# Optimization experiments

Measured on AMD Instinct MI355X. Metric: run time of the kernel, lower is better.

The kernel has to match this reference:

```python
import jax, jax.numpy as jnp
import numpy as np

B, S, D, H = 2, 2048, 1024, 16
DH = D // H  # head_dim = 64


def setup_inputs() -> dict:
    key = jax.random.key(0)
    ks = jax.random.split(key, 12)
    sd = 0.02
    return {
        "query": jax.random.normal(ks[0], (B, S, D), jnp.float32),
        "value": jax.random.normal(ks[1], (B, S, D), jnp.float32),
        "Wq": jax.random.normal(ks[2], (D, D), jnp.float32) * sd,
        "bq": jnp.zeros((D,), jnp.float32),
        "Wk": jax.random.normal(ks[3], (D, DH), jnp.float32) * sd,
        "bk": jnp.zeros((DH,), jnp.float32),
        "Wv": jax.random.normal(ks[4], (D, DH), jnp.float32) * sd,
        "bv": jnp.zeros((DH,), jnp.float32),
        "Wo": jax.random.normal(ks[5], (D, D), jnp.float32) * sd,
        "bo": jnp.zeros((D,), jnp.float32),
    }


def reference(query, value, Wq, bq, Wk, bk, Wv, bv, Wo, bo):
    b, s, d = query.shape
    # per-head queries: (B, H, S, DH)
    Q = (query @ Wq + bq).reshape(b, s, H, DH).transpose(0, 2, 1, 3)
    # single shared K/V head: (B, S, DH)
    K = value @ Wk + bk
    V = value @ Wv + bv
    scale = 1.0 / jnp.sqrt(jnp.asarray(DH, Q.dtype))
    # broadcast shared K over all query heads: (B, H, S, S)
    scores = jnp.einsum("bhsd,btd->bhst", Q, K) * scale
    weights = jax.nn.softmax(scores, axis=-1)
    # (B, H, S, DH)
    attn = jnp.einsum("bhst,btd->bhsd", weights, V)
    concat = attn.transpose(0, 2, 1, 3).reshape(b, s, d)
    return concat @ Wo + bo
```

## Files before the change

### kernel.cpp

```cpp
#include <hip/hip_runtime.h>
#include <hip/hip_bf16.h>
#include <cstdint>

#define S_LEN 2048
#define D_MODEL 1024
#define NHEAD 16
#define DHEAD 64
#define BATCH 2

typedef __attribute__((ext_vector_type(4))) __bf16 bf16x4v;
typedef __attribute__((ext_vector_type(8))) __bf16 bf16x8v;
typedef __attribute__((ext_vector_type(16))) float f32x16;
typedef const __attribute__((address_space(1))) uint32_t gu32;
typedef __attribute__((address_space(3))) uint32_t lu32;

#define QSCALE 0.18033688011112042f

__device__ __forceinline__ int perm4(int gidx) {
    return (gidx & ~3) | ((gidx & 1) << 1) | ((gidx >> 1) & 1);
}
__device__ __forceinline__ int permk(int k) {
    return (k & ~12) | ((k & 4) << 1) | ((k & 8) >> 1);
}

__global__ __launch_bounds__(256) void cvt_f32_bf16(
    const float* __restrict__ in, __hip_bfloat16* __restrict__ out, int n4)
{
    const int i = blockIdx.x * 256 + threadIdx.x;
    if (i < n4) {
        const float4 v = reinterpret_cast<const float4*>(in)[i];
        bf16x4v o = { (__bf16)v.x, (__bf16)v.y, (__bf16)v.z, (__bf16)v.w };
        *reinterpret_cast<bf16x4v*>(out + (size_t)perm4(i) * 4) = o;
    }
}

__global__ __launch_bounds__(256) void wtrans(
    const float* __restrict__ W, __hip_bfloat16* __restrict__ T, int wcols, int trowoff)
{
    __shared__ float ld[32][33];
    const int tid = threadIdx.x;
    const int bx = blockIdx.x, by = blockIdx.y;
    const int jj = tid & 31;
#pragma unroll
    for (int ii = 0; ii < 4; ++ii) {
        const int rr = (tid >> 5) * 4 + ii;
        ld[rr][jj] = W[(size_t)(by * 32 + rr) * wcols + bx * 32 + jj];
    }
    __syncthreads();
#pragma unroll
    for (int ii = 0; ii < 4; ++ii) {
        const int rr = (tid >> 5) * 4 + ii;
        T[(size_t)(trowoff + bx * 32 + rr) * 1024 + by * 32 + permk(jj)] =
            __float2bfloat16(ld[jj][rr]);
    }
}

template<bool FUSED, bool PERMC, typename OutT>
__global__ __launch_bounds__(512, 1) void gemm_mfma(
    const __hip_bfloat16* __restrict__ Ahi, const __hip_bfloat16* __restrict__ Alo,
    const __hip_bfloat16* __restrict__ Bhi,
    const float* __restrict__ bias, OutT* __restrict__ C, float oscale)
{
    constexpr int NT = 16;
    constexpr int LDSZ = FUSED ? 98304 : 65536;
    constexpr int BUFSZ = FUSED ? 49152 : 32768;
    __shared__ __align__(16) char lds[LDSZ];

    const int tid = threadIdx.x;
    const int w = tid >> 6, lane = tid & 63;
    const int g = lane >> 5, r = lane & 31;
    const int wr = w >> 2, wc = w & 3;
    const int lin = blockIdx.y * 8 + blockIdx.x;
    const int swz = (lin & 7) * 32 + (lin >> 3);
    const int rowBase = (swz >> 3) * 128;
    const int colBase = (swz & 7) * 128;

    auto stage = [&](int buf, int t) {
        const int kk = t * 64;
        char* dst = lds + buf * BUFSZ;
#pragma unroll
        for (int j = 0; j < 2; ++j) {
            const int oo  = j * 8192 + tid * 16;
            const int row = oo >> 7;
            const int cb  = (oo & 127) ^ ((row & 7) << 4);
            __builtin_amdgcn_global_load_lds(
                (gu32*)((const char*)Ahi + (size_t)(rowBase + row) * 2048 + kk * 2 + cb),
                (lu32*)(dst + oo), 16, 0, 0);
            if (FUSED)
                __builtin_amdgcn_global_load_lds(
                    (gu32*)((const char*)Alo + (size_t)(rowBase + row) * 2048 + kk * 2 + cb),
                    (lu32*)(dst + 16384 + oo), 16, 0, 0);
            __builtin_amdgcn_global_load_lds(
                (gu32*)((const char*)Bhi + (size_t)(colBase + row) * 2048 + kk * 2 + cb),
                (lu32*)(dst + (FUSED ? 32768 : 16384) + oo), 16, 0, 0);
        }
    };

    f32x16 acc[2];
#pragma unroll
    for (int i = 0; i < 16; ++i) { acc[0][i] = 0.f; acc[1][i] = 0.f; }

    stage(0, 0);

    for (int t = 0; t < NT; ++t) {
        const int cur = t & 1;
        if (t < NT - 1) {
            stage(cur ^ 1, t + 1);
            if (FUSED) { asm volatile("s_waitcnt vmcnt(6)" ::: "memory"); }
            else       { asm volatile("s_waitcnt vmcnt(4)" ::: "memory"); }
        } else {
            asm volatile("s_waitcnt vmcnt(0)" ::: "memory");
        }
        asm volatile("s_barrier" ::: "memory");

        const char* ahb = lds + cur * BUFSZ;
        const char* alb = ahb + 16384;
        const char* bb  = ahb + (FUSED ? 32768 : 16384);

        __builtin_amdgcn_s_setprio(1);
#pragma unroll
        for (int ks = 0; ks < 4; ++ks) {
            bf16x8v a[2], bfr;
#pragma unroll
            for (int mt = 0; mt < 2; ++mt) {
                const int rowl = wr * 64 + mt * 32 + r;
                const int sz = (rowl & 7) << 4;
                a[mt] = *reinterpret_cast<const bf16x8v*>(
                    ahb + rowl * 128 + ((ks * 32 + g * 16) ^ sz));
            }
            {
                const int rowl = wc * 32 + r;
                const int sz = (rowl & 7) << 4;
                bfr = *reinterpret_cast<const bf16x8v*>(
                    bb + rowl * 128 + ((ks * 32 + g * 16) ^ sz));
            }
#pragma unroll
            for (int mt = 0; mt < 2; ++mt)
                acc[mt] = __builtin_amdgcn_mfma_f32_32x32x16_bf16(a[mt], bfr, acc[mt], 0, 0, 0);
            if (FUSED) {
                bf16x8v a2[2];
#pragma unroll
                for (int mt = 0; mt < 2; ++mt) {
                    const int rowl = wr * 64 + mt * 32 + r;
                    const int sz = (rowl & 7) << 4;
                    a2[mt] = *reinterpret_cast<const bf16x8v*>(
                        alb + rowl * 128 + ((ks * 32 + g * 16) ^ sz));
                }
#pragma unroll
                for (int mt = 0; mt < 2; ++mt)
                    acc[mt] = __builtin_amdgcn_mfma_f32_32x32x16_bf16(a2[mt], bfr, acc[mt], 0, 0, 0);
            }
        }
        __builtin_amdgcn_s_setprio(0);
        asm volatile("s_barrier" ::: "memory");
    }

    const int col = colBase + wc * 32 + r;
    const int colp = PERMC ? permk(col) : col;
    const float bv = bias[col];
#pragma unroll
    for (int mt = 0; mt < 2; ++mt)
#pragma unroll
        for (int reg = 0; reg < 16; ++reg) {
            const int row = rowBase + wr * 64 + mt * 32 + (reg & 3) + 8 * (reg >> 2) + 4 * g;
            C[(size_t)row * 1024 + colp] = static_cast<OutT>((acc[mt][reg] + bv) * oscale);
        }
}

__global__ __launch_bounds__(256) void proj_kv_mfma(
    const __hip_bfloat16* __restrict__ Vbf,
    const __hip_bfloat16* __restrict__ Wkvt,
    const float* __restrict__ bk, const float* __restrict__ bv,
    __hip_bfloat16* __restrict__ Kb,
    __hip_bfloat16* __restrict__ Vt)
{
    __shared__ __align__(16) char lds[40960];
    const int tid = threadIdx.x;
    const int w = tid >> 6, lane = tid & 63;
    const int g = lane >> 5, r = lane & 31;
    const int rowBase = blockIdx.x * 32;

    auto stage = [&](int buf, int t) {
        const int kk = t * 64;
        char* dst = lds + buf * 20480;
        {
            const int oo  = tid * 16;
            const int row = oo >> 7;
            const int cb  = (oo & 127) ^ ((row & 7) << 4);
            __builtin_amdgcn_global_load_lds(
                (gu32*)((const char*)Vbf + (size_t)(rowBase + row) * 2048 + kk * 2 + cb),
                (lu32*)(dst + oo), 16, 0, 0);
        }
#pragma unroll
        for (int j = 0; j < 4; ++j) {
            const int oo  = j * 4096 + tid * 16;
            const int row = oo >> 7;
            const int cb  = (oo & 127) ^ ((row & 7) << 4);
            __builtin_amdgcn_global_load_lds(
                (gu32*)((const char*)Wkvt + (size_t)row * 2048 + kk * 2 + cb),
                (lu32*)(dst + 4096 + oo), 16, 0, 0);
        }
    };

    f32x16 acc;
#pragma unroll
    for (int i = 0; i < 16; ++i) acc[i] = 0.f;

    stage(0, 0);

    for (int t = 0; t < 16; ++t) {
        const int cur = t & 1;
        if (t < 15) {
            stage(cur ^ 1, t + 1);
            asm volatile("s_waitcnt vmcnt(5)" ::: "memory");
        } else {
            asm volatile("s_waitcnt vmcnt(0)" ::: "memory");
        }
        asm volatile("s_barrier" ::: "memory");

        const char* ab = lds + cur * 20480;
        const char* bb = ab + 4096;

#pragma unroll
        for (int ks = 0; ks < 4; ++ks) {
            const int sza = (r & 7) << 4;
            bf16x8v af = *reinterpret_cast<const bf16x8v*>(
                ab + r * 128 + ((ks * 32 + g * 16) ^ sza));
            bf16x8v bf = *reinterpret_cast<const bf16x8v*>(
                bb + (w * 32 + r) * 128 + ((ks * 32 + g * 16) ^ sza));
            acc = __builtin_amdgcn_mfma_f32_32x32x16_bf16(af, bf, acc, 0, 0, 0);
        }
        asm volatile("s_barrier" ::: "memory");
    }

    __syncthreads();
    float* ep = reinterpret_cast<float*>(lds);
#pragma unroll
    for (int reg = 0; reg < 16; ++reg) {
        const int m = (reg & 3) + 8 * (reg >> 2) + 4 * g;
        ep[m * 132 + w * 32 + r] = acc[reg];
    }
    __syncthreads();

    {
        const int m  = tid >> 3;
        const int g0 = (tid & 7) * 2;
#pragma unroll
        for (int j = 0; j < 2; ++j) {
            const int gsrc = g0 + j;
            bf16x4v o4;
#pragma unroll
            for (int i2 = 0; i2 < 4; ++i2)
                o4[i2] = (__bf16)(ep[m * 132 + gsrc * 4 + i2] + bk[gsrc * 4 + i2]);
            *reinterpret_cast<bf16x4v*>(
                Kb + (size_t)(rowBase + m) * 64 + perm4(gsrc) * 4) = o4;
        }
    }
    {
        const int vc = tid >> 2;
        const int g0 = (tid & 3) * 2;
        const int batch = rowBase >> 11;
        const float bvv = bv[vc];
#pragma unroll
        for (int j = 0; j < 2; ++j) {
            const int gsrc = g0 + j;
            bf16x4v o4;
#pragma unroll
            for (int i2 = 0; i2 < 4; ++i2)
                o4[i2] = (__bf16)(ep[(gsrc * 4 + i2) * 132 + 64 + vc] + bvv);
            *reinterpret_cast<bf16x4v*>(
                Vt + ((size_t)(batch * 64 + vc)) * 2048 + (rowBase & 2047) + perm4(gsrc) * 4) = o4;
        }
    }
}

__global__ __launch_bounds__(256, 2) void mqa_attn_mfma(
    const __hip_bfloat16* __restrict__ Qbf,
    const __hip_bfloat16* __restrict__ Kbf,
    const __hip_bfloat16* __restrict__ Vt,
    __hip_bfloat16* __restrict__ Ahi,
    __hip_bfloat16* __restrict__ Alo)
{
    __shared__ __align__(16) char lds[65536];

    const int bh = blockIdx.y, b = bh >> 4, h = bh & 15;
    const int qt = blockIdx.x;
    const int tid = threadIdx.x;
    const int w = tid >> 6, lane = tid & 63;
    const int g = lane >> 5, q = lane & 31;

    bf16x8v qf[4];
    {
        const __hip_bfloat16* qp =
            Qbf + ((size_t)(b * S_LEN + qt * 128 + w * 32 + q)) * D_MODEL + h * DHEAD;
#pragma unroll
        for (int ks = 0; ks < 4; ++ks)
            qf[ks] = *reinterpret_cast<const bf16x8v*>(qp + ks * 16 + g * 8);
    }

    const bf16x8v onesf = {(__bf16)1.f, (__bf16)1.f, (__bf16)1.f, (__bf16)1.f,
                           (__bf16)1.f, (__bf16)1.f, (__bf16)1.f, (__bf16)1.f};

    const char* kbase = (const char*)Kbf + (size_t)b * S_LEN * DHEAD * 2;
    const char* vbase = (const char*)Vt + (size_t)b * DHEAD * S_LEN * 2;

    auto stage = [&](int buf, int t0) {
        char* dst = lds + buf * 16384;
#pragma unroll
        for (int j = 0; j < 2; ++j) {
            const int oo = j * 4096 + tid * 16;
            const int rr = oo >> 7;
            const int cc = (oo & 127) ^ ((rr & 7) << 4);
            __builtin_amdgcn_global_load_lds(
                (gu32*)(kbase + (size_t)(t0 + rr) * 128 + cc),
                (lu32*)(dst + oo), 16, 0, 0);
            __builtin_amdgcn_global_load_lds(
                (gu32*)(vbase + (size_t)rr * (S_LEN * 2) + t0 * 2 + cc),
                (lu32*)(dst + 8192 + oo), 16, 0, 0);
        }
    };

    f32x16 oacc[2], oacc_l;
#pragma unroll
    for (int i = 0; i < 16; ++i) { oacc[0][i] = 0.f; oacc[1][i] = 0.f; oacc_l[i] = 0.f; }

    auto qkt = [&](f32x16 (&SD)[2], int buf) {
#pragma unroll
        for (int i = 0; i < 16; ++i) { SD[0][i] = 0.f; SD[1][i] = 0.f; }
        const char* kb_ = lds + buf * 16384;
        __builtin_amdgcn_s_setprio(1);
#pragma unroll
        for (int mt = 0; mt < 2; ++mt) {
            const int key = mt * 32 + q;
            const char* krow = kb_ + key * 128;
            const int swz = (key & 7) << 4;
#pragma unroll
            for (int ks = 0; ks < 4; ++ks) {
                bf16x8v af = *reinterpret_cast<const bf16x8v*>(
                    krow + ((ks * 32 + g * 16) ^ swz));
                SD[mt] = __builtin_amdgcn_mfma_f32_32x32x16_bf16(af, qf[ks], SD[mt], 0, 0, 0);
            }
        }
        __builtin_amdgcn_s_setprio(0);
    };

    auto smpv = [&](f32x16 (&SD)[2], int buf) {
#pragma unroll
        for (int mt = 0; mt < 2; ++mt)
#pragma unroll
            for (int r2 = 0; r2 < 16; ++r2)
                SD[mt][r2] = exp2f(SD[mt][r2]);

        bf16x8v pf[4];
#pragma unroll
        for (int ks = 0; ks < 4; ++ks)
#pragma unroll
            for (int e2 = 0; e2 < 8; ++e2)
                pf[ks][e2] = (__bf16)SD[ks >> 1][(ks & 1) * 8 + e2];

        const char* vb_ = lds + buf * 16384 + 8192;
        __builtin_amdgcn_s_setprio(1);
#pragma unroll
        for (int mt = 0; mt < 2; ++mt) {
            const int drow = mt * 32 + q;
            const char* vrow = vb_ + drow * 128;
            const int swz = (drow & 7) << 4;
#pragma unroll
            for (int ks = 0; ks < 4; ++ks) {
                bf16x8v af = *reinterpret_cast<const bf16x8v*>(
                    vrow + ((ks * 32 + g * 16) ^ swz));
                oacc[mt] = __builtin_amdgcn_mfma_f32_32x32x16_bf16(af, pf[ks], oacc[mt], 0, 0, 0);
            }
        }
#pragma unroll
        for (int ks = 0; ks < 4; ++ks)
            oacc_l = __builtin_amdgcn_mfma_f32_32x32x16_bf16(onesf, pf[ks], oacc_l, 0, 0, 0);
        __builtin_amdgcn_s_setprio(0);
    };

    f32x16 sA[2], sB[2];

    stage(0, 0); stage(1, 64); stage(2, 128);
    asm volatile("s_waitcnt vmcnt(8)" ::: "memory");
    asm volatile("s_barrier" ::: "memory");
    qkt(sA, 0);

#define BODY(SB_, TILE_, BQ_, BP_, CUR, NXT, VMCSTR, DOSTAGE)               \
    {                                                                        \
        asm volatile("s_waitcnt vmcnt(" VMCSTR ")" ::: "memory");            \
        asm volatile("s_barrier" ::: "memory");                              \
        if (DOSTAGE) stage(SB_, TILE_);                                      \
        qkt(NXT, BQ_);                                                       \
        smpv(CUR, BP_);                                                      \
    }

    for (int ib = 0; ib < 7; ++ib) {
        const int t4 = ib * 4;
        BODY(3, (t4 + 3) * 64, 1, 0, sA, sB, "4", true);
        BODY(0, (t4 + 4) * 64, 2, 1, sB, sA, "4", true);
        BODY(1, (t4 + 5) * 64, 3, 2, sA, sB, "4", true);
        BODY(2, (t4 + 6) * 64, 0, 3, sB, sA, "4", true);
    }
    BODY(3, 31 * 64, 1, 0, sA, sB, "4", true);
    BODY(0, 0,       2, 1, sB, sA, "4", false);
    BODY(0, 0,       3, 2, sA, sB, "0", false);
#undef BODY
    smpv(sB, 3);

    const float inv = 1.f / oacc_l[0];
    __syncthreads();
    {
        float* ep = reinterpret_cast<float*>(lds) + w * 2080;
#pragma unroll
        for (int mt = 0; mt < 2; ++mt)
#pragma unroll
            for (int r = 0; r < 16; ++r) {
                const int d = mt * 32 + (r & 3) + ((r >> 2) * 8) + g * 4;
                ep[q * 65 + d] = oacc[mt][r] * inv;
            }
    }
    __syncthreads();

    const size_t obase = (size_t)(b * S_LEN + qt * 128) * D_MODEL + h * DHEAD;
    for (int i = tid; i < 128 * 16; i += 256) {
        const int rloc = i >> 4, G = i & 15;
        const float* src = reinterpret_cast<float*>(lds) + (rloc >> 5) * 2080 + (rloc & 31) * 65 + G * 4;
        const size_t o = obase + (size_t)rloc * D_MODEL + perm4(G) * 4;
        bf16x4v hv, lv;
#pragma unroll
        for (int j = 0; j < 4; ++j) {
            const float v = src[j];
            const float h2 = __bfloat162float(__float2bfloat16(v));
            hv[j] = (__bf16)h2;
            lv[j] = (__bf16)(v - h2);
        }
        *reinterpret_cast<bf16x4v*>(Ahi + o) = hv;
        *reinterpret_cast<bf16x4v*>(Alo + o) = lv;
    }
}

extern "C" void kernel_launch(void* const* d_in, const int* in_sizes, int n_in,
                              void* d_out, int out_size, void* d_ws, size_t ws_size,
                              hipStream_t stream)
{
    const float* query = (const float*)d_in[0];
    const float* value = (const float*)d_in[1];
    const float* Wq    = (const float*)d_in[2];
    const float* bq    = (const float*)d_in[3];
    const float* Wk    = (const float*)d_in[4];
    const float* bk    = (const float*)d_in[5];
    const float* Wv    = (const float*)d_in[6];
    const float* bv    = (const float*)d_in[7];
    const float* Wo    = (const float*)d_in[8];
    const float* bo    = (const float*)d_in[9];
    float* out = (float*)d_out;

    const int BS = BATCH * S_LEN;
    char* ws = (char*)d_ws;
    const size_t MB = 1024 * 1024;
    __hip_bfloat16* Qin   = (__hip_bfloat16*)(ws);
    __hip_bfloat16* AhiB  = (__hip_bfloat16*)(ws);
    __hip_bfloat16* Wqt   = (__hip_bfloat16*)(ws + 8 * MB);
    __hip_bfloat16* Vbf   = (__hip_bfloat16*)(ws + 10 * MB);
    __hip_bfloat16* Qbf   = (__hip_bfloat16*)(ws + 10 * MB);
    __hip_bfloat16* AloB  = (__hip_bfloat16*)(ws + 10 * MB);
    __hip_bfloat16* Kbf   = (__hip_bfloat16*)(ws + 18 * MB);
    __hip_bfloat16* Vt    = (__hip_bfloat16*)(ws + 18 * MB + 524288);
    __hip_bfloat16* Wohit = (__hip_bfloat16*)(ws + 19 * MB);
    __hip_bfloat16* Wkvt  = (__hip_bfloat16*)(ws + 21 * MB);

    cvt_f32_bf16<<<dim3(BS * D_MODEL / 4 / 256), dim3(256), 0, stream>>>(
        query, Qin, BS * D_MODEL / 4);
    cvt_f32_bf16<<<dim3(BS * D_MODEL / 4 / 256), dim3(256), 0, stream>>>(
        value, Vbf, BS * D_MODEL / 4);
    wtrans<<<dim3(32, 32), dim3(256), 0, stream>>>(Wq, Wqt, 1024, 0);
    wtrans<<<dim3(32, 32), dim3(256), 0, stream>>>(Wo, Wohit, 1024, 0);
    wtrans<<<dim3(2, 32), dim3(256), 0, stream>>>(Wk, Wkvt, 64, 0);
    wtrans<<<dim3(2, 32), dim3(256), 0, stream>>>(Wv, Wkvt, 64, 64);

    proj_kv_mfma<<<dim3(BS / 32), dim3(256), 0, stream>>>(Vbf, Wkvt, bk, bv, Kbf, Vt);

    gemm_mfma<false, true, __hip_bfloat16><<<dim3(8, 32), dim3(512), 0, stream>>>(
        Qin, Qin, Wqt, bq, Qbf, QSCALE);

    mqa_attn_mfma<<<dim3(S_LEN / 128, BATCH * NHEAD), dim3(256), 0, stream>>>(
        Qbf, Kbf, Vt, AhiB, AloB);

    gemm_mfma<true, false, float><<<dim3(8, 32), dim3(512), 0, stream>>>(
        AhiB, AloB, Wohit, bo, out, 1.0f);
}
```

Baseline: 124.6 us.

## Merge prep kernels, deepen GEMM LDS pipeline, trim attention QK init and priorities

```diff
diff --git a/kernel.cpp b/kernel.cpp
--- a/kernel.cpp
+++ b/kernel.cpp
@@ -23,23 +23,40 @@
     return (k & ~12) | ((k & 4) << 1) | ((k & 8) >> 1);
 }
 
-__global__ __launch_bounds__(256) void cvt_f32_bf16(
-    const float* __restrict__ in, __hip_bfloat16* __restrict__ out, int n4)
+__global__ __launch_bounds__(256) void prep_cvt(
+    const float* __restrict__ qin, const float* __restrict__ vin,
+    __hip_bfloat16* __restrict__ Qo, __hip_bfloat16* __restrict__ Vo, int n4each)
 {
     const int i = blockIdx.x * 256 + threadIdx.x;
-    if (i < n4) {
-        const float4 v = reinterpret_cast<const float4*>(in)[i];
-        bf16x4v o = { (__bf16)v.x, (__bf16)v.y, (__bf16)v.z, (__bf16)v.w };
-        *reinterpret_cast<bf16x4v*>(out + (size_t)perm4(i) * 4) = o;
-    }
-}
-
-__global__ __launch_bounds__(256) void wtrans(
-    const float* __restrict__ W, __hip_bfloat16* __restrict__ T, int wcols, int trowoff)
+    const float* src;
+    __hip_bfloat16* dst;
+    int idx;
+    if (i < n4each) { src = qin; dst = Qo; idx = i; }
+    else            { src = vin; dst = Vo; idx = i - n4each; if (idx >= n4each) return; }
+    const float4 v = reinterpret_cast<const float4*>(src)[idx];
+    bf16x4v o = { (__bf16)v.x, (__bf16)v.y, (__bf16)v.z, (__bf16)v.w };
+    *reinterpret_cast<bf16x4v*>(dst + (size_t)perm4(idx) * 4) = o;
+}
+
+__global__ __launch_bounds__(256) void wtrans_all(
+    const float* __restrict__ Wq, const float* __restrict__ Wo,
+    const float* __restrict__ Wk, const float* __restrict__ Wv,
+    __hip_bfloat16* __restrict__ Wqt, __hip_bfloat16* __restrict__ Wohit,
+    __hip_bfloat16* __restrict__ Wkvt)
 {
+    const int z = blockIdx.z;
+    const float* W;
+    __hip_bfloat16* T;
+    int wcols, trowoff;
+    if (z == 0)      { W = Wq; T = Wqt;   wcols = 1024; trowoff = 0; }
+    else if (z == 1) { W = Wo; T = Wohit; wcols = 1024; trowoff = 0; }
+    else if (z == 2) { W = Wk; T = Wkvt;  wcols = 64;   trowoff = 0; }
+    else             { W = Wv; T = Wkvt;  wcols = 64;   trowoff = 64; }
+    const int bx = blockIdx.x, by = blockIdx.y;
+    if (bx * 32 >= wcols) return;
+
     __shared__ float ld[32][33];
     const int tid = threadIdx.x;
-    const int bx = blockIdx.x, by = blockIdx.y;
     const int jj = tid & 31;
 #pragma unroll
     for (int ii = 0; ii < 4; ++ii) {
@@ -62,9 +79,9 @@
     const float* __restrict__ bias, OutT* __restrict__ C, float oscale)
 {
     constexpr int NT = 16;
-    constexpr int LDSZ = FUSED ? 98304 : 65536;
+    constexpr int NBUF = FUSED ? 3 : 4;
     constexpr int BUFSZ = FUSED ? 49152 : 32768;
-    __shared__ __align__(16) char lds[LDSZ];
+    __shared__ __align__(16) char lds[NBUF * BUFSZ];
 
     const int tid = threadIdx.x;
     const int w = tid >> 6, lane = tid & 63;
@@ -100,20 +117,27 @@
 #pragma unroll
     for (int i = 0; i < 16; ++i) { acc[0][i] = 0.f; acc[1][i] = 0.f; }
 
-    stage(0, 0);
+    if (FUSED) { stage(0, 0); stage(1, 1); }
+    else       { stage(0, 0); stage(1, 1); stage(2, 2); }
+
+    int b_cur = 0, b_nxt = 1, b_stg = 2;
 
     for (int t = 0; t < NT; ++t) {
-        const int cur = t & 1;
-        if (t < NT - 1) {
-            stage(cur ^ 1, t + 1);
-            if (FUSED) { asm volatile("s_waitcnt vmcnt(6)" ::: "memory"); }
-            else       { asm volatile("s_waitcnt vmcnt(4)" ::: "memory"); }
+        if (FUSED) {
+            if (t < 15) { asm volatile("s_waitcnt vmcnt(6)" ::: "memory"); }
+            else        { asm volatile("s_waitcnt vmcnt(0)" ::: "memory"); }
         } else {
-            asm volatile("s_waitcnt vmcnt(0)" ::: "memory");
+            if (t <= 13)      { asm volatile("s_waitcnt vmcnt(8)" ::: "memory"); }
+            else if (t == 14) { asm volatile("s_waitcnt vmcnt(4)" ::: "memory"); }
+            else              { asm volatile("s_waitcnt vmcnt(0)" ::: "memory"); }
         }
         asm volatile("s_barrier" ::: "memory");
 
-        const char* ahb = lds + cur * BUFSZ;
+        if (FUSED) { if (t + 2 < NT) stage(b_stg, t + 2); }
+        else       { if (t + 3 < NT) stage((t + 3) & 3, t + 3); }
+
+        const int cbuf = FUSED ? b_cur : (t & 3);
+        const char* ahb = lds + cbuf * BUFSZ;
         const char* alb = ahb + 16384;
         const char* bb  = ahb + (FUSED ? 32768 : 16384);
 
@@ -152,7 +176,8 @@
             }
         }
         __builtin_amdgcn_s_setprio(0);
-        asm volatile("s_barrier" ::: "memory");
+
+        if (FUSED) { const int tmp = b_cur; b_cur = b_nxt; b_nxt = b_stg; b_stg = tmp; }
     }
 
     const int col = colBase + wc * 32 + r;
@@ -300,6 +325,9 @@
 
     const bf16x8v onesf = {(__bf16)1.f, (__bf16)1.f, (__bf16)1.f, (__bf16)1.f,
                            (__bf16)1.f, (__bf16)1.f, (__bf16)1.f, (__bf16)1.f};
+    f32x16 fzero;
+#pragma unroll
+    for (int i = 0; i < 16; ++i) fzero[i] = 0.f;
 
     const char* kbase = (const char*)Kbf + (size_t)b * S_LEN * DHEAD * 2;
     const char* vbase = (const char*)Vt + (size_t)b * DHEAD * S_LEN * 2;
@@ -325,23 +353,21 @@
     for (int i = 0; i < 16; ++i) { oacc[0][i] = 0.f; oacc[1][i] = 0.f; oacc_l[i] = 0.f; }
 
     auto qkt = [&](f32x16 (&SD)[2], int buf) {
-#pragma unroll
-        for (int i = 0; i < 16; ++i) { SD[0][i] = 0.f; SD[1][i] = 0.f; }
         const char* kb_ = lds + buf * 16384;
-        __builtin_amdgcn_s_setprio(1);
 #pragma unroll
         for (int mt = 0; mt < 2; ++mt) {
             const int key = mt * 32 + q;
             const char* krow = kb_ + key * 128;
             const int swz = (key & 7) << 4;
-#pragma unroll
-            for (int ks = 0; ks < 4; ++ks) {
+            bf16x8v af0 = *reinterpret_cast<const bf16x8v*>(krow + ((g * 16) ^ swz));
+            SD[mt] = __builtin_amdgcn_mfma_f32_32x32x16_bf16(af0, qf[0], fzero, 0, 0, 0);
+#pragma unroll
+            for (int ks = 1; ks < 4; ++ks) {
                 bf16x8v af = *reinterpret_cast<const bf16x8v*>(
                     krow + ((ks * 32 + g * 16) ^ swz));
                 SD[mt] = __builtin_amdgcn_mfma_f32_32x32x16_bf16(af, qf[ks], SD[mt], 0, 0, 0);
             }
         }
-        __builtin_amdgcn_s_setprio(0);
     };
 
     auto smpv = [&](f32x16 (&SD)[2], int buf) {
@@ -359,7 +385,6 @@
                 pf[ks][e2] = (__bf16)SD[ks >> 1][(ks & 1) * 8 + e2];
 
         const char* vb_ = lds + buf * 16384 + 8192;
-        __builtin_amdgcn_s_setprio(1);
 #pragma unroll
         for (int mt = 0; mt < 2; ++mt) {
             const int drow = mt * 32 + q;
@@ -375,7 +400,6 @@
 #pragma unroll
         for (int ks = 0; ks < 4; ++ks)
             oacc_l = __builtin_amdgcn_mfma_f32_32x32x16_bf16(onesf, pf[ks], oacc_l, 0, 0, 0);
-        __builtin_amdgcn_s_setprio(0);
     };
 
     f32x16 sA[2], sB[2];
@@ -469,14 +493,11 @@
     __hip_bfloat16* Wohit = (__hip_bfloat16*)(ws + 19 * MB);
     __hip_bfloat16* Wkvt  = (__hip_bfloat16*)(ws + 21 * MB);
 
-    cvt_f32_bf16<<<dim3(BS * D_MODEL / 4 / 256), dim3(256), 0, stream>>>(
-        query, Qin, BS * D_MODEL / 4);
-    cvt_f32_bf16<<<dim3(BS * D_MODEL / 4 / 256), dim3(256), 0, stream>>>(
-        value, Vbf, BS * D_MODEL / 4);
-    wtrans<<<dim3(32, 32), dim3(256), 0, stream>>>(Wq, Wqt, 1024, 0);
-    wtrans<<<dim3(32, 32), dim3(256), 0, stream>>>(Wo, Wohit, 1024, 0);
-    wtrans<<<dim3(2, 32), dim3(256), 0, stream>>>(Wk, Wkvt, 64, 0);
-    wtrans<<<dim3(2, 32), dim3(256), 0, stream>>>(Wv, Wkvt, 64, 64);
+    const int n4each = BS * D_MODEL / 4;
+    prep_cvt<<<dim3(2 * n4each / 256), dim3(256), 0, stream>>>(
+        query, value, Qin, Vbf, n4each);
+    wtrans_all<<<dim3(32, 32, 4), dim3(256), 0, stream>>>(
+        Wq, Wo, Wk, Wv, Wqt, Wohit, Wkvt);
 
     proj_kv_mfma<<<dim3(BS / 32), dim3(256), 0, stream>>>(Vbf, Wkvt, bk, bv, Kbf, Vt);
 
```

Measured after the change: 114.5 us. -8.2%, faster.
